# Optimization experiments

Hardware: AMD Instinct MI355X
Metric: run time of the kernel (lower is better)

## Reference

```python
import jax, jax.numpy as jnp
import numpy as np

BATCH = 32768
HIDDEN = 512
OUT = 2
FUTURE_STEPS = 60


def _lstm_cell(x, h, c, w_ih, w_hh, b_ih, b_hh):
    # PyTorch gate order: i, f, g, o
    g = x @ w_ih.T + h @ w_hh.T + b_ih + b_hh
    i, f, gg, o = jnp.split(g, 4, axis=-1)
    c_new = jax.nn.sigmoid(f) * c + jax.nn.sigmoid(i) * jnp.tanh(gg)
    h_new = jax.nn.sigmoid(o) * jnp.tanh(c_new)
    return h_new, c_new


def setup_inputs() -> dict:
    key = jax.random.key(0)
    ks = jax.random.split(key, 16)
    s = 0.05
    inp = {
        "h": jax.random.normal(ks[0], (BATCH, HIDDEN), jnp.float32),
        "w_init_h": jax.random.normal(ks[1], (HIDDEN, HIDDEN), jnp.float32) * s,
        "b_init_h": jax.random.normal(ks[2], (HIDDEN,), jnp.float32) * s,
        "w_init_c": jax.random.normal(ks[3], (HIDDEN, HIDDEN), jnp.float32) * s,
        "b_init_c": jax.random.normal(ks[4], (HIDDEN,), jnp.float32) * s,
        "w_ih0": jax.random.normal(ks[5], (4 * HIDDEN, OUT), jnp.float32) * s,
        "w_hh0": jax.random.normal(ks[6], (4 * HIDDEN, HIDDEN), jnp.float32) * s,
        "b_ih0": jax.random.normal(ks[7], (4 * HIDDEN,), jnp.float32) * s,
        "b_hh0": jax.random.normal(ks[8], (4 * HIDDEN,), jnp.float32) * s,
        "w_ih1": jax.random.normal(ks[9], (4 * HIDDEN, HIDDEN), jnp.float32) * s,
        "w_hh1": jax.random.normal(ks[10], (4 * HIDDEN, HIDDEN), jnp.float32) * s,
        "b_ih1": jax.random.normal(ks[11], (4 * HIDDEN,), jnp.float32) * s,
        "b_hh1": jax.random.normal(ks[12], (4 * HIDDEN,), jnp.float32) * s,
        "w_out": jax.random.normal(ks[13], (OUT, HIDDEN), jnp.float32) * s,
        "b_out": jax.random.normal(ks[14], (OUT,), jnp.float32) * s,
    }
    return inp


def reference(h, w_init_h, b_init_h, w_init_c, b_init_c,
              w_ih0, w_hh0, b_ih0, b_hh0,
              w_ih1, w_hh1, b_ih1, b_hh1,
              w_out, b_out):
    batch = h.shape[0]
    # same initial (h, c) replicated to both LSTM layers (repeat(2,1,1))
    h0 = h @ w_init_h.T + b_init_h
    c0 = h @ w_init_c.T + b_init_c
    x0 = jnp.zeros((batch, OUT), h.dtype)

    def step(carry, _):
        x, h1, c1, h2, c2 = carry
        h1, c1 = _lstm_cell(x, h1, c1, w_ih0, w_hh0, b_ih0, b_hh0)
        h2, c2 = _lstm_cell(h1, h2, c2, w_ih1, w_hh1, b_ih1, b_hh1)
        pred = h2 @ w_out.T + b_out  # [batch, OUT]
        return (pred, h1, c1, h2, c2), pred

    _, preds = jax.lax.scan(step, (x0, h0, c0, h0, c0), None, length=FUTURE_STEPS)
    return jnp.transpose(preds, (1, 0, 2))  # [batch, future_steps, OUT]
```

## Files before the change

### kernel.cpp

```cpp
#include <hip/hip_runtime.h>

#define HID    512
#define TPB    512
#define NSTEP  60
#define BMI    64

using f32x4 = __attribute__((ext_vector_type(4))) float;
using s16x8 = __attribute__((ext_vector_type(8))) short;

__device__ __forceinline__ unsigned short f2bf(float f) {
    unsigned u = __builtin_bit_cast(unsigned, f);
    u += 0x7fffu + ((u >> 16) & 1u);
    return (unsigned short)(u >> 16);
}
__device__ __forceinline__ float bf2f(unsigned u) {
    return __builtin_bit_cast(float, u << 16);
}
__device__ __forceinline__ float sigm(float x) { return 1.0f / (1.0f + __expf(-x)); }
__device__ __forceinline__ float tanh_(float x) { return 1.0f - 2.0f / (__expf(2.0f * x) + 1.0f); }

__global__ void pack_kernel(const float* __restrict__ w_hh0, const float* __restrict__ w_ih1,
                            const float* __restrict__ w_hh1, const float* __restrict__ w_init_h,
                            const float* __restrict__ w_init_c,
                            const float* __restrict__ b_ih0, const float* __restrict__ b_hh0,
                            const float* __restrict__ b_ih1, const float* __restrict__ b_hh1,
                            unsigned short* __restrict__ PW1, unsigned short* __restrict__ PW2,
                            unsigned short* __restrict__ PI,
                            float* __restrict__ b1, float* __restrict__ b2)
{
    int idx = blockIdx.x * 256 + threadIdx.x;
    if (idx < 1048576) {
        int el = idx & 511, fr = idx >> 9;
        int ks = fr & 15, ct = (fr >> 4) & 7, s = fr >> 7;
        int lane = el >> 3, e = el & 7;
        int l15 = lane & 15;
        int gcol = (l15 & 3) * 512 + s * 32 + ct * 4 + (l15 >> 2);
        int k = ks * 32 + (lane >> 4) * 8 + e;
        PW1[idx] = f2bf(w_hh0[gcol * 512 + k]);
        return;
    }
    int i2 = idx - 1048576;
    if (i2 >= 0 && i2 < 2097152) {
        int el = i2 & 511, fr = i2 >> 9;
        int ks = fr & 31, ct = (fr >> 5) & 7, s = fr >> 8;
        int lane = el >> 3, e = el & 7;
        int l15 = lane & 15;
        int gcol = (l15 & 3) * 512 + s * 32 + ct * 4 + (l15 >> 2);
        int kk = (ks & 15) * 32 + (lane >> 4) * 8 + e;
        float v = (ks < 16) ? w_ih1[gcol * 512 + kk] : w_hh1[gcol * 512 + kk];
        PW2[i2] = f2bf(v);
        return;
    }
    int i3 = idx - (1048576 + 2097152);
    if (i3 >= 0 && i3 < 524288) {
        int el = i3 & 511, fr = i3 >> 9;
        int ks = fr & 15, tile = fr >> 4;
        int s = tile >> 5, c = tile & 31;
        int lane = el >> 3, e = el & 7;
        int n = c * 16 + (lane & 15);
        int k = ks * 32 + (lane >> 4) * 8 + e;
        float v = s ? w_init_c[n * 512 + k] : w_init_h[n * 512 + k];
        PI[i3] = f2bf(v);
        return;
    }
    int i4 = idx - (1048576 + 2097152 + 524288);
    if (i4 >= 0 && i4 < 2048) b1[i4] = b_ih0[i4] + b_hh0[i4];
    else if (i4 >= 2048 && i4 < 4096) b2[i4 - 2048] = b_ih1[i4 - 2048] + b_hh1[i4 - 2048];
}

__global__ __launch_bounds__(TPB, 2) void init_kernel(
    const float* __restrict__ hin, const unsigned short* __restrict__ PI,
    const float* __restrict__ b_init_h, const float* __restrict__ b_init_c,
    unsigned short* __restrict__ h1s, unsigned short* __restrict__ h2s,
    unsigned short* __restrict__ c1s, unsigned short* __restrict__ c2s)
{
    __shared__ unsigned short bufA[BMI * HID];
    const int tid = threadIdx.x, lane = tid & 63, wave = tid >> 6;
    const int m0 = blockIdx.x * BMI;
    const int l15 = lane & 15, lg = lane >> 4;
    const int swz = (lane & 7) << 4;

    for (int j = 0; j < 16; ++j) {
        int e = tid * 4 + j * 2048;
        int row = e >> 9, col = e & 511;
        float4 v = *(const float4*)(hin + (size_t)(m0 + row) * HID + col);
        ushort4 w;
        w.x = f2bf(v.x); w.y = f2bf(v.y); w.z = f2bf(v.z); w.w = f2bf(v.w);
        int L = (row * 1024 + col * 2) ^ ((row & 7) << 4);
        *(ushort4*)((char*)bufA + L) = w;
    }
    __syncthreads();

    #pragma unroll 1
    for (int cc = 0; cc < 4; ++cc) {
        int c = wave * 4 + cc;
        int nc = c * 16 + l15;
        f32x4 acc[4][2];
        #pragma unroll
        for (int rt = 0; rt < 4; ++rt)
            #pragma unroll
            for (int s = 0; s < 2; ++s)
                #pragma unroll
                for (int r = 0; r < 4; ++r) acc[rt][s][r] = 0.0f;

        #pragma unroll
        for (int ks = 0; ks < 16; ++ks) {
            s16x8 a[4];
            #pragma unroll
            for (int rt = 0; rt < 4; ++rt) {
                int ao = (rt * 16 + l15) * 1024 + ((ks * 64 + lg * 16) ^ swz);
                a[rt] = *(const s16x8*)((const char*)bufA + ao);
            }
            #pragma unroll
            for (int s = 0; s < 2; ++s) {
                s16x8 b = ((const s16x8*)PI)[((s * 32 + c) * 16 + ks) * 64 + lane];
                #pragma unroll
                for (int rt = 0; rt < 4; ++rt)
                    acc[rt][s] = __builtin_amdgcn_mfma_f32_16x16x32_bf16(a[rt], b, acc[rt][s], 0, 0, 0);
            }
        }
        float bh = b_init_h[nc], bc = b_init_c[nc];
        #pragma unroll
        for (int rt = 0; rt < 4; ++rt)
            #pragma unroll
            for (int r = 0; r < 4; ++r) {
                int m = m0 + rt * 16 + lg * 4 + r;
                float hv = acc[rt][0][r] + bh;
                float cv = acc[rt][1][r] + bc;
                unsigned short hb = f2bf(hv);
                size_t o = (size_t)m * HID + nc;
                h1s[o] = hb; h2s[o] = hb;
                c1s[o] = f2bf(cv); c2s[o] = f2bf(cv);
            }
    }
}

__global__ __launch_bounds__(TPB, 2) void l1_kernel(
    const unsigned short* __restrict__ h1R, unsigned short* __restrict__ h1W,
    unsigned short* __restrict__ c1s, const float* __restrict__ pp,
    float* __restrict__ outp, const unsigned short* __restrict__ PW1,
    const float* __restrict__ b1, const float* __restrict__ w_ih0,
    const float* __restrict__ b_out, int t)
{
    __shared__ __align__(16) unsigned short Ab[2 * 16384];
    __shared__ __align__(16) float xls[4096];
    __shared__ __align__(16) float tsc[8 * 320];

    const int tid = threadIdx.x, lane = tid & 63, w = tid >> 6;
    const int b = blockIdx.x;
    const int g = 2 * (b & 7) + (b >> 7);
    const int s = (b >> 3) & 15;
    const int m0 = g * 2048;
    const int l15 = lane & 15, lg = lane >> 4;
    const int q = l15 & 3, a = l15 >> 2;
    const int ct = w;
    const int hid = s * 32 + ct * 4 + a;
    float* const ts = tsc + w * 320;

    s16x8 bw[16];
    #pragma unroll
    for (int ks = 0; ks < 16; ++ks)
        bw[ks] = ((const s16x8*)PW1)[((s * 8 + ct) * 16 + ks) * 64 + lane];

    float b1v[4], wiA[4], wiB[4];
    #pragma unroll
    for (int k = 0; k < 4; ++k) {
        int gc = k * 512 + hid;
        b1v[k] = b1[gc];
        wiA[k] = w_ih0[gc * 2 + 0];
        wiB[k] = w_ih0[gc * 2 + 1];
    }
    float bo0 = b_out[0], bo1 = b_out[1];

    if (t == 0) {
        #pragma unroll
        for (int i = 0; i < 8; ++i) xls[tid * 8 + i] = 0.0f;
    } else {
        f32x4 s0 = {0.f,0.f,0.f,0.f}, s1 = {0.f,0.f,0.f,0.f};
        #pragma unroll 1
        for (int ss = 0; ss < 16; ++ss) {
            const float* p = pp + (((size_t)(g * 16 + ss)) << 12) + tid * 8;
            s0 += *(const f32x4*)p;
            s1 += *(const f32x4*)(p + 4);
        }
        s0[0] += bo0; s0[1] += bo1; s0[2] += bo0; s0[3] += bo1;
        s1[0] += bo0; s1[1] += bo1; s1[2] += bo0; s1[3] += bo1;
        *(f32x4*)(xls + tid * 8) = s0;
        *(f32x4*)(xls + tid * 8 + 4) = s1;
        if (s == 0) {
            float* ob = outp + (size_t)(m0 + tid * 4) * (2 * NSTEP) + (t - 1) * 2;
            *(float2*)(ob)             = make_float2(s0[0], s0[1]);
            *(float2*)(ob + 2 * NSTEP) = make_float2(s0[2], s0[3]);
            *(float2*)(ob + 4 * NSTEP) = make_float2(s1[0], s1[1]);
            *(float2*)(ob + 6 * NSTEP) = make_float2(s1[2], s1[3]);
        }
    }

    const int st_l15 = tid & 15, st_lg = (tid >> 4) & 3, st_rh = (tid >> 6) & 1, st_kq = tid >> 7;
    const int st_grow = st_rh * 16 + st_l15;

    uint4 nv[4];
    #pragma unroll
    for (int p = 0; p < 4; ++p) {
        int ks = p * 4 + st_kq;
        uint4 v = *(const uint4*)(h1R + (size_t)(m0 + st_grow) * HID + ks * 32 + st_lg * 8);
        *(uint4*)((char*)Ab + p * 8192 + tid * 16) = v;
    }
    #pragma unroll
    for (int p = 0; p < 4; ++p) {
        int ks = p * 4 + st_kq;
        nv[p] = *(const uint4*)(h1R + (size_t)(m0 + 32 + st_grow) * HID + ks * 32 + st_lg * 8);
    }
    unsigned short cpr0 = c1s[(size_t)(m0 + lg * 4 + q) * HID + hid];
    unsigned short cpr1 = c1s[(size_t)(m0 + 16 + lg * 4 + q) * HID + hid];
    __syncthreads();

    #pragma unroll 1
    for (int ch = 0; ch < 64; ++ch) {
        if (ch < 63) {
            char* AbW = (char*)Ab + ((ch + 1) & 1) * 32768;
            #pragma unroll
            for (int p = 0; p < 4; ++p)
                *(uint4*)(AbW + p * 8192 + tid * 16) = nv[p];
        }
        if (ch < 62) {
            #pragma unroll
            for (int p = 0; p < 4; ++p) {
                int ks = p * 4 + st_kq;
                nv[p] = *(const uint4*)(h1R + (size_t)(m0 + (ch + 2) * 32 + st_grow) * HID + ks * 32 + st_lg * 8);
            }
        }
        unsigned short cnx0 = 0, cnx1 = 0;
        if (ch < 63) {
            cnx0 = c1s[(size_t)(m0 + (ch + 1) * 32 + lg * 4 + q) * HID + hid];
            cnx1 = c1s[(size_t)(m0 + (ch + 1) * 32 + 16 + lg * 4 + q) * HID + hid];
        }

        const char* AbR = (const char*)Ab + (ch & 1) * 32768;
        f32x4 a0A = {0.f,0.f,0.f,0.f}, a0B = {0.f,0.f,0.f,0.f};
        f32x4 a1A = {0.f,0.f,0.f,0.f}, a1B = {0.f,0.f,0.f,0.f};
        #pragma unroll
        for (int ksl = 0; ksl < 8; ++ksl) {
            s16x8 x0 = *(const s16x8*)(AbR + ksl * 2048 + lane * 16);
            s16x8 x1 = *(const s16x8*)(AbR + ksl * 2048 + 1024 + lane * 16);
            a0A = __builtin_amdgcn_mfma_f32_16x16x32_bf16(x0, bw[ksl], a0A, 0, 0, 0);
            a1A = __builtin_amdgcn_mfma_f32_16x16x32_bf16(x1, bw[ksl], a1A, 0, 0, 0);
        }
        #pragma unroll
        for (int ksl = 8; ksl < 16; ++ksl) {
            s16x8 x0 = *(const s16x8*)(AbR + ksl * 2048 + lane * 16);
            s16x8 x1 = *(const s16x8*)(AbR + ksl * 2048 + 1024 + lane * 16);
            a0B = __builtin_amdgcn_mfma_f32_16x16x32_bf16(x0, bw[ksl], a0B, 0, 0, 0);
            a1B = __builtin_amdgcn_mfma_f32_16x16x32_bf16(x1, bw[ksl], a1B, 0, 0, 0);
        }
        f32x4 acS0 = a0A + a0B, acS1 = a1A + a1B;

        #pragma unroll
        for (int rh = 0; rh < 2; ++rh) {
            f32x4 ac = rh ? acS1 : acS0;
            #pragma unroll
            for (int r = 0; r < 4; ++r)
                ts[(lg * 4 + r) * 20 + l15] = ac[r];
            f32x4 gq = *(const f32x4*)(ts + (lg * 4 + q) * 20 + a * 4);

            int grow = ch * 32 + rh * 16 + lg * 4 + q;
            float2 xv = *(const float2*)(xls + grow * 2);
            float iv = sigm(gq[0] + b1v[0] + xv.x * wiA[0] + xv.y * wiB[0]);
            float fv = sigm(gq[1] + b1v[1] + xv.x * wiA[1] + xv.y * wiB[1]);
            float gv = tanh_(gq[2] + b1v[2] + xv.x * wiA[2] + xv.y * wiB[2]);
            float ov = sigm(gq[3] + b1v[3] + xv.x * wiA[3] + xv.y * wiB[3]);
            float cold = bf2f(rh ? cpr1 : cpr0);
            float cn = fv * cold + iv * gv;
            float hn = ov * tanh_(cn);
            size_t cix = (size_t)(m0 + grow) * HID + hid;
            c1s[cix] = f2bf(cn);
            h1W[cix] = f2bf(hn);
        }
        cpr0 = cnx0; cpr1 = cnx1;
        __syncthreads();
    }
}

__global__ __launch_bounds__(TPB, 2) void l2_kernel(
    const unsigned short* __restrict__ h1C, const unsigned short* __restrict__ h2R,
    unsigned short* __restrict__ h2W, unsigned short* __restrict__ c2s,
    float* __restrict__ pp,
    const unsigned short* __restrict__ PW2, const float* __restrict__ b2,
    const float* __restrict__ w_out)
{
    __shared__ __align__(16) unsigned short Ab[2 * 32768];
    __shared__ __align__(16) float pl[2][32][2][9];
    __shared__ __align__(16) float tsc[8 * 320];

    const int tid = threadIdx.x, lane = tid & 63, w = tid >> 6;
    const int b = blockIdx.x;
    const int g = 2 * (b & 7) + (b >> 7);
    const int s = (b >> 3) & 15;
    const int m0 = g * 2048;
    const int l15 = lane & 15, lg = lane >> 4;
    const int q = l15 & 3, a = l15 >> 2;
    const int ct = w;
    const int hid = s * 32 + ct * 4 + a;
    float* const ts = tsc + w * 320;

    s16x8 bw[32];
    #pragma unroll
    for (int ks = 0; ks < 32; ++ks)
        bw[ks] = ((const s16x8*)PW2)[((s * 8 + ct) * 32 + ks) * 64 + lane];

    float b2v[4];
    #pragma unroll
    for (int k = 0; k < 4; ++k) b2v[k] = b2[k * 512 + hid];
    const float wo0 = w_out[hid], wo1 = w_out[512 + hid];

    const int st_l15 = tid & 15, st_lg = (tid >> 4) & 3, st_rh = (tid >> 6) & 1, st_kq = tid >> 7;
    const int st_grow = st_rh * 16 + st_l15;

    uint4 nv[8];
    #pragma unroll
    for (int p = 0; p < 8; ++p) {
        int ks = p * 4 + st_kq;
        const unsigned short* src = (ks < 16) ? h1C : h2R;
        int kel = (ks < 16) ? ks : (ks - 16);
        uint4 v = *(const uint4*)(src + (size_t)(m0 + st_grow) * HID + kel * 32 + st_lg * 8);
        *(uint4*)((char*)Ab + p * 8192 + tid * 16) = v;
    }
    #pragma unroll
    for (int p = 0; p < 8; ++p) {
        int ks = p * 4 + st_kq;
        const unsigned short* src = (ks < 16) ? h1C : h2R;
        int kel = (ks < 16) ? ks : (ks - 16);
        nv[p] = *(const uint4*)(src + (size_t)(m0 + 32 + st_grow) * HID + kel * 32 + st_lg * 8);
    }
    unsigned short cpr0 = c2s[(size_t)(m0 + lg * 4 + q) * HID + hid];
    unsigned short cpr1 = c2s[(size_t)(m0 + 16 + lg * 4 + q) * HID + hid];
    __syncthreads();

    #pragma unroll 1
    for (int ch = 0; ch < 64; ++ch) {
        if (ch < 63) {
            char* AbW = (char*)Ab + ((ch + 1) & 1) * 65536;
            #pragma unroll
            for (int p = 0; p < 8; ++p)
                *(uint4*)(AbW + p * 8192 + tid * 16) = nv[p];
        }
        if (ch < 62) {
            #pragma unroll
            for (int p = 0; p < 8; ++p) {
                int ks = p * 4 + st_kq;
                const unsigned short* src = (ks < 16) ? h1C : h2R;
                int kel = (ks < 16) ? ks : (ks - 16);
                nv[p] = *(const uint4*)(src + (size_t)(m0 + (ch + 2) * 32 + st_grow) * HID + kel * 32 + st_lg * 8);
            }
        }
        unsigned short cnx0 = 0, cnx1 = 0;
        if (ch < 63) {
            cnx0 = c2s[(size_t)(m0 + (ch + 1) * 32 + lg * 4 + q) * HID + hid];
            cnx1 = c2s[(size_t)(m0 + (ch + 1) * 32 + 16 + lg * 4 + q) * HID + hid];
        }

        const char* AbR = (const char*)Ab + (ch & 1) * 65536;
        f32x4 a0A = {0.f,0.f,0.f,0.f}, a0B = {0.f,0.f,0.f,0.f};
        f32x4 a1A = {0.f,0.f,0.f,0.f}, a1B = {0.f,0.f,0.f,0.f};
        #pragma unroll
        for (int ksl = 0; ksl < 16; ++ksl) {
            s16x8 x0 = *(const s16x8*)(AbR + ksl * 2048 + lane * 16);
            s16x8 x1 = *(const s16x8*)(AbR + ksl * 2048 + 1024 + lane * 16);
            a0A = __builtin_amdgcn_mfma_f32_16x16x32_bf16(x0, bw[ksl], a0A, 0, 0, 0);
            a1A = __builtin_amdgcn_mfma_f32_16x16x32_bf16(x1, bw[ksl], a1A, 0, 0, 0);
        }
        #pragma unroll
        for (int ksl = 16; ksl < 32; ++ksl) {
            s16x8 x0 = *(const s16x8*)(AbR + ksl * 2048 + lane * 16);
            s16x8 x1 = *(const s16x8*)(AbR + ksl * 2048 + 1024 + lane * 16);
            a0B = __builtin_amdgcn_mfma_f32_16x16x32_bf16(x0, bw[ksl], a0B, 0, 0, 0);
            a1B = __builtin_amdgcn_mfma_f32_16x16x32_bf16(x1, bw[ksl], a1B, 0, 0, 0);
        }
        f32x4 acS0 = a0A + a0B, acS1 = a1A + a1B;

        #pragma unroll
        for (int rh = 0; rh < 2; ++rh) {
            f32x4 ac = rh ? acS1 : acS0;
            #pragma unroll
            for (int r = 0; r < 4; ++r)
                ts[(lg * 4 + r) * 20 + l15] = ac[r];
            f32x4 gq = *(const f32x4*)(ts + (lg * 4 + q) * 20 + a * 4);

            int rloc = rh * 16 + lg * 4 + q;
            int grow = ch * 32 + rloc;
            float iv = sigm(gq[0] + b2v[0]);
            float fv = sigm(gq[1] + b2v[1]);
            float gv = tanh_(gq[2] + b2v[2]);
            float ov = sigm(gq[3] + b2v[3]);
            float cold = bf2f(rh ? cpr1 : cpr0);
            float cn = fv * cold + iv * gv;
            float hn = ov * tanh_(cn);
            size_t cix = (size_t)(m0 + grow) * HID + hid;
            c2s[cix] = f2bf(cn);
            h2W[cix] = f2bf(hn);
            float p0 = hn * wo0, p1 = hn * wo1;
            p0 += __shfl_xor(p0, 4); p0 += __shfl_xor(p0, 8);
            p1 += __shfl_xor(p1, 4); p1 += __shfl_xor(p1, 8);
            if (a == 0) {
                pl[ch & 1][rloc][0][ct] = p0;
                pl[ch & 1][rloc][1][ct] = p1;
            }
        }
        if (ch > 0 && tid < 64) {
            int row = tid >> 1, j = tid & 1;
            const float* pr = &pl[(ch - 1) & 1][row][j][0];
            float sum = pr[0] + pr[1] + pr[2] + pr[3] + pr[4] + pr[5] + pr[6] + pr[7];
            pp[((size_t)(g * 16 + s)) * 4096 + (size_t)((ch - 1) * 32 + row) * 2 + j] = sum;
        }
        cpr0 = cnx0; cpr1 = cnx1;
        __syncthreads();
    }
    if (tid < 64) {
        int row = tid >> 1, j = tid & 1;
        const float* pr = &pl[1][row][j][0];
        float sum = pr[0] + pr[1] + pr[2] + pr[3] + pr[4] + pr[5] + pr[6] + pr[7];
        pp[((size_t)(g * 16 + s)) * 4096 + (size_t)(63 * 32 + row) * 2 + j] = sum;
    }
}

__global__ void tail_kernel(const float* __restrict__ pp, const float* __restrict__ b_out,
                            float* __restrict__ outp)
{
    int i = blockIdx.x * 256 + threadIdx.x;
    if (i < 65536) {
        int m = i >> 1, j = i & 1;
        int g = m >> 11;
        int idx = (m & 2047) * 2 + j;
        float sum = b_out[j];
        #pragma unroll 1
        for (int s = 0; s < 16; ++s)
            sum += pp[(((size_t)(g * 16 + s)) << 12) + idx];
        outp[(size_t)m * (2 * NSTEP) + (NSTEP - 1) * 2 + j] = sum;
    }
}

extern "C" void kernel_launch(void* const* d_in, const int* in_sizes, int n_in,
                              void* d_out, int out_size, void* d_ws, size_t ws_size,
                              hipStream_t stream)
{
    (void)in_sizes; (void)n_in; (void)out_size; (void)ws_size;
    const float* h        = (const float*)d_in[0];
    const float* w_init_h = (const float*)d_in[1];
    const float* b_init_h = (const float*)d_in[2];
    const float* w_init_c = (const float*)d_in[3];
    const float* b_init_c = (const float*)d_in[4];
    const float* w_ih0    = (const float*)d_in[5];
    const float* w_hh0    = (const float*)d_in[6];
    const float* b_ih0    = (const float*)d_in[7];
    const float* b_hh0    = (const float*)d_in[8];
    const float* w_ih1    = (const float*)d_in[9];
    const float* w_hh1    = (const float*)d_in[10];
    const float* b_ih1    = (const float*)d_in[11];
    const float* b_hh1    = (const float*)d_in[12];
    const float* w_out    = (const float*)d_in[13];
    const float* b_out    = (const float*)d_in[14];
    float* out = (float*)d_out;

    char* ws = (char*)d_ws;
    unsigned short* h1s[2] = { (unsigned short*)(ws + 0),
                               (unsigned short*)(ws + 33554432) };
    unsigned short* h2s[2] = { (unsigned short*)(ws + 67108864),
                               (unsigned short*)(ws + 100663296) };
    unsigned short* c1s = (unsigned short*)(ws + 134217728);
    unsigned short* c2s = (unsigned short*)(ws + 167772160);
    float* pp           = (float*)(ws + 201326592);
    unsigned short* PW1 = (unsigned short*)(ws + 205520896);
    unsigned short* PW2 = (unsigned short*)(ws + 207618048);
    unsigned short* PI  = (unsigned short*)(ws + 211812352);
    float* b1 = (float*)(ws + 212860928);
    float* b2 = (float*)(ws + 212869120);

    pack_kernel<<<14352, 256, 0, stream>>>(w_hh0, w_ih1, w_hh1, w_init_h, w_init_c,
                                           b_ih0, b_hh0, b_ih1, b_hh1, PW1, PW2, PI, b1, b2);
    init_kernel<<<32768 / BMI, TPB, 0, stream>>>(h, PI, b_init_h, b_init_c,
                                                 h1s[1], h2s[1], c1s, c2s);
    for (int t = 0; t < NSTEP; ++t) {
        const unsigned short* h1R = h1s[(t + 1) & 1];
        unsigned short* h1W = h1s[t & 1];
        const unsigned short* h2R = h2s[(t + 1) & 1];
        unsigned short* h2W = h2s[t & 1];
        l1_kernel<<<256, TPB, 0, stream>>>(h1R, h1W, c1s, pp, out, PW1, b1, w_ih0, b_out, t);
        l2_kernel<<<256, TPB, 0, stream>>>(h1W, h2R, h2W, c2s, pp, PW2, b2, w_out);
    }
    tail_kernel<<<256, 256, 0, stream>>>(pp, b_out, out);
}
```

Baseline: 38.21 ms.

## Tile hidden/cell state buffers into per-block contiguous 2048x32 regions

Changes the global layout of the h and c state buffers from row-major [batch][512] to regions of 2048 rows by 32 columns, one per (batch group, hidden slice), padded to a custom stride. Each block's c reads and h/c writes become contiguous within its own region rather than strided by 512 elements. The shared-memory staging addresses are remapped to match the new load pattern. The padded stride is meant to avoid channel or bank camping, at the cost of a slightly larger workspace and more complex index math.

```diff
diff --git a/kernel.cpp b/kernel.cpp
--- a/kernel.cpp
+++ b/kernel.cpp
@@ -4,6 +4,7 @@
 #define TPB    512
 #define NSTEP  60
 #define BMI    64
+#define RSTRIDE 65664
 
 using f32x4 = __attribute__((ext_vector_type(4))) float;
 using s16x8 = __attribute__((ext_vector_type(8))) short;
@@ -128,7 +129,8 @@
                 float hv = acc[rt][0][r] + bh;
                 float cv = acc[rt][1][r] + bc;
                 unsigned short hb = f2bf(hv);
-                size_t o = (size_t)m * HID + nc;
+                size_t o = (size_t)((m >> 11) * 16 + (nc >> 5)) * RSTRIDE
+                         + (size_t)(m & 2047) * 32 + (nc & 31);
                 h1s[o] = hb; h2s[o] = hb;
                 c1s[o] = f2bf(cv); c2s[o] = f2bf(cv);
             }
@@ -156,6 +158,8 @@
     const int ct = w;
     const int hid = s * 32 + ct * 4 + a;
     float* const ts = tsc + w * 320;
+    const size_t myReg = (size_t)(g * 16 + s) * RSTRIDE;
+    const int myCol = ct * 4 + a;
 
     s16x8 bw[16];
     #pragma unroll
@@ -196,23 +200,25 @@
         }
     }
 
-    const int st_l15 = tid & 15, st_lg = (tid >> 4) & 3, st_rh = (tid >> 6) & 1, st_kq = tid >> 7;
-    const int st_grow = st_rh * 16 + st_l15;
+    const int st_ks4 = tid >> 7;
+    const int st_row = (tid >> 2) & 31;
+    const int st_lgq = tid & 3;
+    const size_t gR = (size_t)(g * 16);
 
     uint4 nv[4];
     #pragma unroll
     for (int p = 0; p < 4; ++p) {
-        int ks = p * 4 + st_kq;
-        uint4 v = *(const uint4*)(h1R + (size_t)(m0 + st_grow) * HID + ks * 32 + st_lg * 8);
-        *(uint4*)((char*)Ab + p * 8192 + tid * 16) = v;
+        int ks = p * 4 + st_ks4;
+        uint4 v = *(const uint4*)(h1R + (gR + ks) * RSTRIDE + (size_t)st_row * 32 + st_lgq * 8);
+        *(uint4*)((char*)Ab + ks * 2048 + (st_row >> 4) * 1024 + st_lgq * 256 + (st_row & 15) * 16) = v;
     }
     #pragma unroll
     for (int p = 0; p < 4; ++p) {
-        int ks = p * 4 + st_kq;
-        nv[p] = *(const uint4*)(h1R + (size_t)(m0 + 32 + st_grow) * HID + ks * 32 + st_lg * 8);
-    }
-    unsigned short cpr0 = c1s[(size_t)(m0 + lg * 4 + q) * HID + hid];
-    unsigned short cpr1 = c1s[(size_t)(m0 + 16 + lg * 4 + q) * HID + hid];
+        int ks = p * 4 + st_ks4;
+        nv[p] = *(const uint4*)(h1R + (gR + ks) * RSTRIDE + (size_t)(32 + st_row) * 32 + st_lgq * 8);
+    }
+    unsigned short cpr0 = c1s[myReg + (size_t)(lg * 4 + q) * 32 + myCol];
+    unsigned short cpr1 = c1s[myReg + (size_t)(16 + lg * 4 + q) * 32 + myCol];
     __syncthreads();
 
     #pragma unroll 1
@@ -220,20 +226,22 @@
         if (ch < 63) {
             char* AbW = (char*)Ab + ((ch + 1) & 1) * 32768;
             #pragma unroll
-            for (int p = 0; p < 4; ++p)
-                *(uint4*)(AbW + p * 8192 + tid * 16) = nv[p];
+            for (int p = 0; p < 4; ++p) {
+                int ks = p * 4 + st_ks4;
+                *(uint4*)(AbW + ks * 2048 + (st_row >> 4) * 1024 + st_lgq * 256 + (st_row & 15) * 16) = nv[p];
+            }
         }
         if (ch < 62) {
             #pragma unroll
             for (int p = 0; p < 4; ++p) {
-                int ks = p * 4 + st_kq;
-                nv[p] = *(const uint4*)(h1R + (size_t)(m0 + (ch + 2) * 32 + st_grow) * HID + ks * 32 + st_lg * 8);
+                int ks = p * 4 + st_ks4;
+                nv[p] = *(const uint4*)(h1R + (gR + ks) * RSTRIDE + (size_t)((ch + 2) * 32 + st_row) * 32 + st_lgq * 8);
             }
         }
         unsigned short cnx0 = 0, cnx1 = 0;
         if (ch < 63) {
-            cnx0 = c1s[(size_t)(m0 + (ch + 1) * 32 + lg * 4 + q) * HID + hid];
-            cnx1 = c1s[(size_t)(m0 + (ch + 1) * 32 + 16 + lg * 4 + q) * HID + hid];
+            cnx0 = c1s[myReg + (size_t)((ch + 1) * 32 + lg * 4 + q) * 32 + myCol];
+            cnx1 = c1s[myReg + (size_t)((ch + 1) * 32 + 16 + lg * 4 + q) * 32 + myCol];
         }
 
         const char* AbR = (const char*)Ab + (ch & 1) * 32768;
@@ -272,7 +280,7 @@
             float cold = bf2f(rh ? cpr1 : cpr0);
             float cn = fv * cold + iv * gv;
             float hn = ov * tanh_(cn);
-            size_t cix = (size_t)(m0 + grow) * HID + hid;
+            size_t cix = myReg + (size_t)grow * 32 + myCol;
             c1s[cix] = f2bf(cn);
             h1W[cix] = f2bf(hn);
         }
@@ -296,12 +304,13 @@
     const int b = blockIdx.x;
     const int g = 2 * (b & 7) + (b >> 7);
     const int s = (b >> 3) & 15;
-    const int m0 = g * 2048;
     const int l15 = lane & 15, lg = lane >> 4;
     const int q = l15 & 3, a = l15 >> 2;
     const int ct = w;
     const int hid = s * 32 + ct * 4 + a;
     float* const ts = tsc + w * 320;
+    const size_t myReg = (size_t)(g * 16 + s) * RSTRIDE;
+    const int myCol = ct * 4 + a;
 
     s16x8 bw[32];
     #pragma unroll
@@ -313,27 +322,29 @@
     for (int k = 0; k < 4; ++k) b2v[k] = b2[k * 512 + hid];
     const float wo0 = w_out[hid], wo1 = w_out[512 + hid];
 
-    const int st_l15 = tid & 15, st_lg = (tid >> 4) & 3, st_rh = (tid >> 6) & 1, st_kq = tid >> 7;
-    const int st_grow = st_rh * 16 + st_l15;
+    const int st_ks4 = tid >> 7;
+    const int st_row = (tid >> 2) & 31;
+    const int st_lgq = tid & 3;
+    const size_t gR = (size_t)(g * 16);
 
     uint4 nv[8];
     #pragma unroll
     for (int p = 0; p < 8; ++p) {
-        int ks = p * 4 + st_kq;
+        int ks = p * 4 + st_ks4;
         const unsigned short* src = (ks < 16) ? h1C : h2R;
         int kel = (ks < 16) ? ks : (ks - 16);
-        uint4 v = *(const uint4*)(src + (size_t)(m0 + st_grow) * HID + kel * 32 + st_lg * 8);
-        *(uint4*)((char*)Ab + p * 8192 + tid * 16) = v;
+        uint4 v = *(const uint4*)(src + (gR + kel) * RSTRIDE + (size_t)st_row * 32 + st_lgq * 8);
+        *(uint4*)((char*)Ab + ks * 2048 + (st_row >> 4) * 1024 + st_lgq * 256 + (st_row & 15) * 16) = v;
     }
     #pragma unroll
     for (int p = 0; p < 8; ++p) {
-        int ks = p * 4 + st_kq;
+        int ks = p * 4 + st_ks4;
         const unsigned short* src = (ks < 16) ? h1C : h2R;
         int kel = (ks < 16) ? ks : (ks - 16);
-        nv[p] = *(const uint4*)(src + (size_t)(m0 + 32 + st_grow) * HID + kel * 32 + st_lg * 8);
-    }
-    unsigned short cpr0 = c2s[(size_t)(m0 + lg * 4 + q) * HID + hid];
-    unsigned short cpr1 = c2s[(size_t)(m0 + 16 + lg * 4 + q) * HID + hid];
+        nv[p] = *(const uint4*)(src + (gR + kel) * RSTRIDE + (size_t)(32 + st_row) * 32 + st_lgq * 8);
+    }
+    unsigned short cpr0 = c2s[myReg + (size_t)(lg * 4 + q) * 32 + myCol];
+    unsigned short cpr1 = c2s[myReg + (size_t)(16 + lg * 4 + q) * 32 + myCol];
     __syncthreads();
 
     #pragma unroll 1
@@ -341,22 +352,24 @@
         if (ch < 63) {
             char* AbW = (char*)Ab + ((ch + 1) & 1) * 65536;
             #pragma unroll
-            for (int p = 0; p < 8; ++p)
-                *(uint4*)(AbW + p * 8192 + tid * 16) = nv[p];
+            for (int p = 0; p < 8; ++p) {
+                int ks = p * 4 + st_ks4;
+                *(uint4*)(AbW + ks * 2048 + (st_row >> 4) * 1024 + st_lgq * 256 + (st_row & 15) * 16) = nv[p];
+            }
         }
         if (ch < 62) {
             #pragma unroll
             for (int p = 0; p < 8; ++p) {
-                int ks = p * 4 + st_kq;
+                int ks = p * 4 + st_ks4;
                 const unsigned short* src = (ks < 16) ? h1C : h2R;
                 int kel = (ks < 16) ? ks : (ks - 16);
-                nv[p] = *(const uint4*)(src + (size_t)(m0 + (ch + 2) * 32 + st_grow) * HID + kel * 32 + st_lg * 8);
+                nv[p] = *(const uint4*)(src + (gR + kel) * RSTRIDE + (size_t)((ch + 2) * 32 + st_row) * 32 + st_lgq * 8);
             }
         }
         unsigned short cnx0 = 0, cnx1 = 0;
         if (ch < 63) {
-            cnx0 = c2s[(size_t)(m0 + (ch + 1) * 32 + lg * 4 + q) * HID + hid];
-            cnx1 = c2s[(size_t)(m0 + (ch + 1) * 32 + 16 + lg * 4 + q) * HID + hid];
+            cnx0 = c2s[myReg + (size_t)((ch + 1) * 32 + lg * 4 + q) * 32 + myCol];
+            cnx1 = c2s[myReg + (size_t)((ch + 1) * 32 + 16 + lg * 4 + q) * 32 + myCol];
         }
 
         const char* AbR = (const char*)Ab + (ch & 1) * 65536;
@@ -395,7 +408,7 @@
             float cold = bf2f(rh ? cpr1 : cpr0);
             float cn = fv * cold + iv * gv;
             float hn = ov * tanh_(cn);
-            size_t cix = (size_t)(m0 + grow) * HID + hid;
+            size_t cix = myReg + (size_t)grow * 32 + myCol;
             c2s[cix] = f2bf(cn);
             h2W[cix] = f2bf(hn);
             float p0 = hn * wo0, p1 = hn * wo1;
@@ -461,19 +474,21 @@
     const float* b_out    = (const float*)d_in[14];
     float* out = (float*)d_out;
 
+    const size_t SREG = (size_t)256 * RSTRIDE * 2;
     char* ws = (char*)d_ws;
-    unsigned short* h1s[2] = { (unsigned short*)(ws + 0),
-                               (unsigned short*)(ws + 33554432) };
-    unsigned short* h2s[2] = { (unsigned short*)(ws + 67108864),
-                               (unsigned short*)(ws + 100663296) };
-    unsigned short* c1s = (unsigned short*)(ws + 134217728);
-    unsigned short* c2s = (unsigned short*)(ws + 167772160);
-    float* pp           = (float*)(ws + 201326592);
-    unsigned short* PW1 = (unsigned short*)(ws + 205520896);
-    unsigned short* PW2 = (unsigned short*)(ws + 207618048);
-    unsigned short* PI  = (unsigned short*)(ws + 211812352);
-    float* b1 = (float*)(ws + 212860928);
-    float* b2 = (float*)(ws + 212869120);
+    unsigned short* h1s[2] = { (unsigned short*)(ws + 0 * SREG),
+                               (unsigned short*)(ws + 1 * SREG) };
+    unsigned short* h2s[2] = { (unsigned short*)(ws + 2 * SREG),
+                               (unsigned short*)(ws + 3 * SREG) };
+    unsigned short* c1s = (unsigned short*)(ws + 4 * SREG);
+    unsigned short* c2s = (unsigned short*)(ws + 5 * SREG);
+    char* tail = ws + 6 * SREG;
+    float* pp           = (float*)(tail);
+    unsigned short* PW1 = (unsigned short*)(tail + 4194304);
+    unsigned short* PW2 = (unsigned short*)(tail + 6291456);
+    unsigned short* PI  = (unsigned short*)(tail + 10485760);
+    float* b1 = (float*)(tail + 11534336);
+    float* b2 = (float*)(tail + 11542528);
 
     pack_kernel<<<14352, 256, 0, stream>>>(w_hh0, w_ih1, w_hh1, w_init_h, w_init_c,
                                            b_ih0, b_hh0, b_ih1, b_hh1, PW1, PW2, PI, b1, b2);
```

New measurement: 40.48 ms. 5.9% more time.
